# Kernel tuning notes

Measured on AMD Instinct MI355X. Metric: run time of the kernel, lower is better.

The kernel has to match this reference:

```python
import jax, jax.numpy as jnp
import numpy as np

M = 64            # multiplicity of 0e and of 1e irreps
NM = 2 * M        # num_mul = 128
SQ3 = float(np.sqrt(3.0))
SQ6 = float(np.sqrt(6.0))
C0 = float(np.sqrt(1.0 / 5.0))   # path weight for 0e outputs: sqrt(dim_out=1 / n_paths=5)
C1 = float(np.sqrt(3.0 / 5.0))   # path weight for 1e outputs: sqrt(dim_out=3 / n_paths=5)


def split_irreps(x):
    # x: [..., 256] -> scalars [..., 64], vectors [..., 64, 3]
    return x[:, :M], x[:, M:].reshape(x.shape[0], M, 3)


def merge_irreps(s, v):
    return jnp.concatenate([s, v.reshape(v.shape[0], -1)], axis=-1)


def o3_linear(x, W0, b0, W1):
    # e3nn o3.Linear: per-l mixing across multiplicities, shared over m, 1/sqrt(fan_in) norm, bias only on 0e
    s, v = split_irreps(x)
    s = s @ W0 / jnp.sqrt(jnp.float32(M)) + b0
    v = jnp.einsum('nuc,uv->nvc', v, W1) / jnp.sqrt(jnp.float32(M))
    return merge_irreps(s, v)


def ssp(x):
    return jax.nn.softplus(x) - jnp.log(2.0)


def norm_gate(x, W1, b1, W2, b2):
    # NormGate: gate 1e channels by MLP of [scalars, per-channel norms]
    s, v = split_irreps(x)
    nrm = jnp.sqrt(jnp.sum(v * v, axis=-1))             # [E, M]
    f0 = jnp.concatenate([s, nrm], axis=-1)             # [E, 2M]
    g = jax.nn.silu(f0 @ W1 + b1) @ W2 + b2             # [E, 2M]
    return merge_irreps(g[:, :M], v * g[:, M:, None])


def tp_node_pair(x, y, w):
    # weighted 'uuu' tensor product, instructions: (0e,0e->0e), (0e,1e->1e), (1e,0e->1e), (1e,1e->0e), (1e,1e->1e)
    xs, xv = split_irreps(x)
    ys, yv = split_irreps(y)
    w000, w011, w101, w110, w111 = jnp.split(w, 5, axis=-1)   # each [E, M]
    out_s = C0 * (w000 * xs * ys + w110 * jnp.sum(xv * yv, -1) / SQ3)
    out_v = C1 * (w011[..., None] * xs[..., None] * yv / SQ3
                  + w101[..., None] * xv * ys[..., None] / SQ3
                  + w111[..., None] * jnp.cross(xv, yv) / SQ6)
    return merge_irreps(out_s, out_v)


def reference(node_attr, edge_attr, node_pair_attr, Wi0, bi0, Wi1, gpW1, gpb1, gpW2, gpb2,
              Wn0, bn0, Wn1, feW1, feW2, fsW1, fsb1, fsW2, fsb2,
              gW1, gb1, gW2, gb2, Wo0, bo0, Wo1, edge_index):
    dst, src = edge_index[0], edge_index[1]
    # --- invariant branch: per-edge scalar descriptor s0 ---
    na0 = o3_linear(node_attr, Wi0, bi0, Wi1)
    s_d, v_d = split_irreps(na0[dst])
    s_s, v_s = split_irreps(na0[src])
    ip = jnp.sum(v_d * v_s, axis=-1) / 3.0               # InnerProduct of 1e channels (1/ir.dim)
    s0 = jnp.concatenate([s_d, s_s, ip], axis=-1)        # [E, 3M]
    # --- node feature branch ---
    h = norm_gate(node_attr, gpW1, gpb1, gpW2, gpb2)
    h = o3_linear(h, Wn0, bn0, Wn1)
    # --- edge-conditioned TP weights ---
    fe = ssp(edge_attr @ feW1 / jnp.sqrt(32.0)) @ feW2 / jnp.sqrt(8.0)   # FullyConnectedNet, [E, 5M]
    fs = jax.nn.silu(s0 @ fsW1 + fsb1) @ fsW2 + fsb2                     # [E, 5M]
    w = fe * fs
    # --- pair message ---
    pair = tp_node_pair(h[src], h[dst], w)
    pair = norm_gate(pair, gW1, gb1, gW2, gb2)
    pair = o3_linear(pair, Wo0, bo0, Wo1)
    return pair + node_pair_attr


def setup_inputs():
    key = jax.random.key(0)
    ks = jax.random.split(key, 20)
    N, E, EA, WN = 20000, 120000, 32, 320
    f32 = jnp.float32
    def nrm(k, shape, scale=1.0):
        return jax.random.normal(k, shape, dtype=f32) * scale
    return {
        'node_attr': nrm(ks[0], (N, 4 * M)),
        'edge_attr': nrm(ks[1], (E, EA)),
        'node_pair_attr': nrm(ks[2], (E, 4 * M)),
        'Wi0': nrm(ks[3], (M, M)), 'bi0': jnp.zeros((M,), f32), 'Wi1': nrm(ks[4], (M, M)),
        'gpW1': nrm(ks[5], (NM, NM), 1.0 / np.sqrt(NM)), 'gpb1': jnp.zeros((NM,), f32),
        'gpW2': nrm(ks[6], (NM, NM), 1.0 / np.sqrt(NM)), 'gpb2': jnp.zeros((NM,), f32),
        'Wn0': nrm(ks[7], (M, M)), 'bn0': jnp.zeros((M,), f32), 'Wn1': nrm(ks[8], (M, M)),
        'feW1': nrm(ks[9], (EA, 8)), 'feW2': nrm(ks[10], (8, WN)),
        'fsW1': nrm(ks[11], (3 * M, M), 1.0 / np.sqrt(3 * M)), 'fsb1': jnp.zeros((M,), f32),
        'fsW2': nrm(ks[12], (M, WN), 1.0 / np.sqrt(M)), 'fsb2': jnp.zeros((WN,), f32),
        'gW1': nrm(ks[13], (NM, NM), 1.0 / np.sqrt(NM)), 'gb1': jnp.zeros((NM,), f32),
        'gW2': nrm(ks[14], (NM, NM), 1.0 / np.sqrt(NM)), 'gb2': jnp.zeros((NM,), f32),
        'Wo0': nrm(ks[15], (M, M)), 'bo0': jnp.zeros((M,), f32), 'Wo1': nrm(ks[16], (M, M)),
        'edge_index': jax.random.randint(ks[17], (2, E), 0, N, dtype=jnp.int32),
    }
```

## Files before the change

kernel.cpp:

```cpp
#include <hip/hip_runtime.h>
#include <hip/hip_bf16.h>
#include <math.h>


static __device__ __forceinline__ float siluf(float x) { return x / (1.f + __expf(-x)); }
static __device__ __forceinline__ float sspf(float x) {
  return fmaxf(x, 0.f) + log1pf(__expf(-fabsf(x))) - 0.6931471805599453f;
}
static __device__ __forceinline__ short f2b(float x) {
  __hip_bfloat16 b = __float2bfloat16(x);
  short s; __builtin_memcpy(&s, &b, 2); return s;
}
static __device__ __forceinline__ float b2f(short s) {
  unsigned int u = ((unsigned int)(unsigned short)s) << 16;
  float f; __builtin_memcpy(&f, &u, 4); return f;
}

typedef __attribute__((ext_vector_type(4))) short short4v;
typedef __attribute__((ext_vector_type(8))) short short8v;
typedef __attribute__((ext_vector_type(16))) float f32x16;

static __device__ __forceinline__ short8v ld8(const short* p) {
  const short4v* q = (const short4v*)p;
  short4v a = q[0], b = q[1];
  short8v r;
  r[0] = a[0]; r[1] = a[1]; r[2] = a[2]; r[3] = a[3];
  r[4] = b[0]; r[5] = b[1]; r[6] = b[2]; r[7] = b[3];
  return r;
}

static __device__ __forceinline__ short8v gld8(const short* __restrict__ p) {
  return *reinterpret_cast<const short8v*>(p);
}

static __device__ __forceinline__ void sp2(short* hp, short* lp, float x) {
  short hh = f2b(x); *hp = hh; *lp = f2b(x - b2f(hh));
}

#define WOFF_FSW1 0
#define WOFF_FSW2 12288
#define WOFF_FEW1 32768
#define WOFF_FEW2 33792
#define WOFF_GW1  38912
#define WOFF_GW2  55296
#define WOFF_WO0  71680
#define WOFF_WO1  75776
#define NOFF_WI0  79872
#define NOFF_WI1  88064
#define NOFF_GP1  96256
#define NOFF_GP2  129024
#define NOFF_WN0  161792
#define NOFF_WN1  169984
#define W_ALL     178176

__global__ __launch_bounds__(256) void prep_weights(
    const float* __restrict__ fsW1, const float* __restrict__ fsW2,
    const float* __restrict__ feW1, const float* __restrict__ feW2,
    const float* __restrict__ gW1, const float* __restrict__ gW2,
    const float* __restrict__ Wo0, const float* __restrict__ Wo1,
    const float* __restrict__ Wi0, const float* __restrict__ Wi1,
    const float* __restrict__ gpW1, const float* __restrict__ gpW2,
    const float* __restrict__ Wn0, const float* __restrict__ Wn1,
    short* __restrict__ wsb)
{
  const int gt = blockIdx.x * blockDim.x + threadIdx.x;
  const int gs = gridDim.x * blockDim.x;
  for (int i = gt; i < 12288; i += gs) { int k = (i >> 10) * 16 + (i & 15), n = (i >> 4) & 63;  wsb[WOFF_FSW1 + i] = f2b(fsW1[k * 64 + n]); }
  for (int i = gt; i < 20480; i += gs) { int k = (i / 5120) * 16 + (i & 15), n = (i >> 4) % 320; wsb[WOFF_FSW2 + i] = f2b(fsW2[k * 320 + n]); }
  for (int i = gt; i < 1024; i += gs)  { int k = (i >> 9) * 16 + (i & 15),  n = (i >> 4) & 31;  wsb[WOFF_FEW1 + i] = (n < 8) ? f2b(feW1[k * 8 + n]) : 0; }
  for (int i = gt; i < 5120; i += gs)  { int k = i & 15,                    n = (i >> 4) % 320; wsb[WOFF_FEW2 + i] = (k < 8) ? f2b(feW2[k * 320 + n]) : 0; }
  for (int i = gt; i < 16384; i += gs) { int k = (i >> 11) * 16 + (i & 15), n = (i >> 4) & 127; wsb[WOFF_GW1 + i] = f2b(gW1[k * 128 + n]); }
  for (int i = gt; i < 16384; i += gs) { int k = (i >> 11) * 16 + (i & 15), n = (i >> 4) & 127; wsb[WOFF_GW2 + i] = f2b(gW2[k * 128 + n]); }
  for (int i = gt; i < 4096; i += gs)  { int k = (i >> 10) * 16 + (i & 15), n = (i >> 4) & 63;  wsb[WOFF_WO0 + i] = f2b(Wo0[k * 64 + n]); }
  for (int i = gt; i < 4096; i += gs)  { int k = (i >> 10) * 16 + (i & 15), n = (i >> 4) & 63;  wsb[WOFF_WO1 + i] = f2b(Wo1[k * 64 + n]); }
  for (int i = gt; i < 4096; i += gs)  { int k = (i >> 10) * 16 + (i & 15), n = (i >> 4) & 63;  float w = Wi0[k * 64 + n];  short hh = f2b(w); wsb[NOFF_WI0 + i] = hh; wsb[NOFF_WI0 + 4096 + i] = f2b(w - b2f(hh)); }
  for (int i = gt; i < 4096; i += gs)  { int k = (i >> 10) * 16 + (i & 15), n = (i >> 4) & 63;  float w = Wi1[k * 64 + n];  short hh = f2b(w); wsb[NOFF_WI1 + i] = hh; wsb[NOFF_WI1 + 4096 + i] = f2b(w - b2f(hh)); }
  for (int i = gt; i < 16384; i += gs) { int k = (i >> 11) * 16 + (i & 15), n = (i >> 4) & 127; float w = gpW1[k * 128 + n]; short hh = f2b(w); wsb[NOFF_GP1 + i] = hh; wsb[NOFF_GP1 + 16384 + i] = f2b(w - b2f(hh)); }
  for (int i = gt; i < 16384; i += gs) { int k = (i >> 11) * 16 + (i & 15), n = (i >> 4) & 127; float w = gpW2[k * 128 + n]; short hh = f2b(w); wsb[NOFF_GP2 + i] = hh; wsb[NOFF_GP2 + 16384 + i] = f2b(w - b2f(hh)); }
  for (int i = gt; i < 4096; i += gs)  { int k = (i >> 10) * 16 + (i & 15), n = (i >> 4) & 63;  float w = Wn0[k * 64 + n];  short hh = f2b(w); wsb[NOFF_WN0 + i] = hh; wsb[NOFF_WN0 + 4096 + i] = f2b(w - b2f(hh)); }
  for (int i = gt; i < 4096; i += gs)  { int k = (i >> 10) * 16 + (i & 15), n = (i >> 4) & 63;  float w = Wn1[k * 64 + n];  short hh = f2b(w); wsb[NOFF_WN1 + i] = hh; wsb[NOFF_WN1 + 4096 + i] = f2b(w - b2f(hh)); }
}

#define MFMA32(a, b, c) __builtin_amdgcn_mfma_f32_32x32x16_bf16(a, b, c, 0, 0, 0)

#define MFMA_HL(ah, al, bh, bl, acc) \
  do { acc = MFMA32((al), (bh), acc); acc = MFMA32((ah), (bl), acc); acc = MFMA32((ah), (bh), acc); } while (0)

#define XS_H 0
#define V0H  4352
#define F0H  17408
#define F0L  21632
#define TBH  0
#define TBL  4224
#define GVH  8704
#define GSH  21760
#define GSL  23936
#define NODE_LDS_SHORTS 26112

__global__ __launch_bounds__(256, 2) void node_kernel(
    const float* __restrict__ na,
    const float* __restrict__ bi0, const float* __restrict__ gpb1,
    const float* __restrict__ gpb2, const float* __restrict__ bn0,
    const short* __restrict__ wsb,
    float* __restrict__ na0, float* __restrict__ h, int N)
{
  __shared__ __align__(16) short smem[NODE_LDS_SHORTS];
  const int tid = threadIdx.x;
  const int wv = tid >> 6, ln = tid & 63;
  const int m32 = ln & 31, kh = ln >> 5;
  const int nb0 = blockIdx.x * 32;

  for (int i = 0; i < 8; ++i) {
    const int e = wv * 8 + i;
    int ng = nb0 + e; if (ng >= N) ng = N - 1;
    const float* xp = na + (size_t)ng * 256;
    const int u = ln;
    const float xs = xp[u];
    const float v0 = xp[64 + 3 * u], v1 = xp[64 + 3 * u + 1], v2 = xp[64 + 3 * u + 2];
    const float nr = sqrtf(v0 * v0 + v1 * v1 + v2 * v2);
    sp2(smem + XS_H + e * 68 + u,        smem + XS_H + 2176 + e * 68 + u, xs);
    sp2(smem + V0H + 0 * 4352 + e * 68 + u, smem + V0H + 0 * 4352 + 2176 + e * 68 + u, v0);
    sp2(smem + V0H + 1 * 4352 + e * 68 + u, smem + V0H + 1 * 4352 + 2176 + e * 68 + u, v1);
    sp2(smem + V0H + 2 * 4352 + e * 68 + u, smem + V0H + 2 * 4352 + 2176 + e * 68 + u, v2);
    sp2(smem + F0H + e * 132 + u,        smem + F0L + e * 132 + u, xs);
    sp2(smem + F0H + e * 132 + 64 + u,   smem + F0L + e * 132 + 64 + u, nr);
  }
  __syncthreads();

  {
    const int g = wv;
    const short* Ah = smem + (g == 0 ? XS_H : V0H + (g - 1) * 4352) + m32 * 68 + kh * 8;
    const short* Al = Ah + 2176;
    const int bofs = (g == 0) ? NOFF_WI0 : NOFF_WI1;
    for (int nt = 0; nt < 2; ++nt) {
      f32x16 acc = {};
      const int n = nt * 32 + m32;
      const short* Bh = wsb + bofs + n * 16 + kh * 8;
      const short* Bl = Bh + 4096;
#pragma unroll 2
      for (int k0 = 0; k0 < 4; ++k0) {
        short8v ah = ld8(Ah + k0 * 16), al = ld8(Al + k0 * 16);
        short8v bh = gld8(Bh + k0 * 1024), bl = gld8(Bl + k0 * 1024);
        MFMA_HL(ah, al, bh, bl, acc);
      }
      const float bias = (g == 0) ? bi0[n] : 0.f;
      const int off = (g == 0) ? n : 64 + 3 * n + (g - 1);
#pragma unroll
      for (int r = 0; r < 16; ++r) {
        int row = (r & 3) + 8 * (r >> 2) + 4 * kh;
        int ng = nb0 + row;
        if (ng < N) na0[(size_t)ng * 256 + off] = acc[r] * 0.125f + bias;
      }
    }
  }
  __syncthreads();

  {
    f32x16 acc = {};
    const int n = wv * 32 + m32;
    const short* Ah = smem + F0H + m32 * 132 + kh * 8;
    const short* Al = smem + F0L + m32 * 132 + kh * 8;
    const short* Bh = wsb + NOFF_GP1 + n * 16 + kh * 8;
    const short* Bl = Bh + 16384;
#pragma unroll 2
    for (int k0 = 0; k0 < 8; ++k0) {
      short8v ah = ld8(Ah + k0 * 16), al = ld8(Al + k0 * 16);
      short8v bh = gld8(Bh + k0 * 2048), bl = gld8(Bl + k0 * 2048);
      MFMA_HL(ah, al, bh, bl, acc);
    }
    const float bias = gpb1[n];
#pragma unroll
    for (int r = 0; r < 16; ++r) {
      int row = (r & 3) + 8 * (r >> 2) + 4 * kh;
      float t = siluf(acc[r] + bias);
      sp2(smem + TBH + row * 132 + n, smem + TBL + row * 132 + n, t);
    }
  }
  __syncthreads();

  {
    f32x16 acc = {};
    const int n = wv * 32 + m32;
    const short* Ah = smem + TBH + m32 * 132 + kh * 8;
    const short* Al = smem + TBL + m32 * 132 + kh * 8;
    const short* Bh = wsb + NOFF_GP2 + n * 16 + kh * 8;
    const short* Bl = Bh + 16384;
#pragma unroll 2
    for (int k0 = 0; k0 < 8; ++k0) {
      short8v ah = ld8(Ah + k0 * 16), al = ld8(Al + k0 * 16);
      short8v bh = gld8(Bh + k0 * 2048), bl = gld8(Bl + k0 * 2048);
      MFMA_HL(ah, al, bh, bl, acc);
    }
    const float bias = gpb2[n];
#pragma unroll
    for (int r = 0; r < 16; ++r) {
      int row = (r & 3) + 8 * (r >> 2) + 4 * kh;
      float val = acc[r] + bias;
      if (wv < 2) {
        sp2(smem + GSH + row * 68 + n, smem + GSL + row * 68 + n, val);
      } else {
        const int u = n - 64;
        int ng = nb0 + row; if (ng >= N) ng = N - 1;
        const float* vp = na + (size_t)ng * 256 + 64 + 3 * u;
#pragma unroll
        for (int c = 0; c < 3; ++c) {
          float pv = vp[c] * val;
          sp2(smem + GVH + c * 4352 + row * 68 + u,
              smem + GVH + c * 4352 + 2176 + row * 68 + u, pv);
        }
      }
    }
  }
  __syncthreads();

  {
    const int g = wv;
    const short* Ah = smem + (g == 0 ? GSH : GVH + (g - 1) * 4352) + m32 * 68 + kh * 8;
    const short* Al = Ah + 2176;
    const int bofs = (g == 0) ? NOFF_WN0 : NOFF_WN1;
    for (int nt = 0; nt < 2; ++nt) {
      f32x16 acc = {};
      const int n = nt * 32 + m32;
      const short* Bh = wsb + bofs + n * 16 + kh * 8;
      const short* Bl = Bh + 4096;
#pragma unroll 2
      for (int k0 = 0; k0 < 4; ++k0) {
        short8v ah = ld8(Ah + k0 * 16), al = ld8(Al + k0 * 16);
        short8v bh = gld8(Bh + k0 * 1024), bl = gld8(Bl + k0 * 1024);
        MFMA_HL(ah, al, bh, bl, acc);
      }
      const float bias = (g == 0) ? bn0[n] : 0.f;
      const int off = (g == 0) ? n : 64 + 3 * n + (g - 1);
#pragma unroll
      for (int r = 0; r < 16; ++r) {
        int row = (r & 3) + 8 * (r >> 2) + 4 * kh;
        int ng = nb0 + row;
        if (ng < N) h[(size_t)ng * 256 + off] = acc[r] * 0.125f + bias;
      }
    }
  }
}

#define A_HIDE  0
#define A_HID2  640
#define A_S0    2816
#define A_EA    9088
#define A_WB    2816
#define A_F0    13056
#define A_PV    17280
#define A_TB    2816
#define A_GATED 7040
#define ACT_TOTAL 23424
#define LDS_BYTES (ACT_TOTAL * 2)

__global__ __launch_bounds__(256, 3) void edge_kernel(
    const float* __restrict__ ea,
    const float* __restrict__ npa,
    const float* __restrict__ fsb1, const float* __restrict__ fsb2,
    const float* __restrict__ gb1, const float* __restrict__ gb2,
    const float* __restrict__ bo0,
    const int* __restrict__ eidx,
    const float* __restrict__ na0, const float* __restrict__ h,
    const short* __restrict__ wsb,
    float* __restrict__ out, int E)
{
  extern __shared__ __align__(16) short smem[];
  short* hidEb  = smem + A_HIDE;
  short* hid2b  = smem + A_HID2;
  short* s0b    = smem + A_S0;
  short* earowb = smem + A_EA;
  short* wb     = smem + A_WB;
  short* f0b    = smem + A_F0;
  short* pvb    = smem + A_PV;
  short* tb     = smem + A_TB;
  short* gated  = smem + A_GATED;

  const int tid = threadIdx.x;
  const int wv = tid >> 6, ln = tid & 63;
  const int m32 = ln & 31, kh = ln >> 5;
  const int e0 = blockIdx.x * 32;

  const float C0c = 0.4472135954999579f;
  const float C1c = 0.7745966692414834f;
  const float iS3 = 0.5773502691896258f;
  const float iS6 = 0.40824829046386307f;
  const float isq32 = 0.17677669529663687f;
  const float isq8 = 0.35355339059327373f;

  for (int i = tid; i < 32 * 32; i += 256) {
    int e = i >> 5, k = i & 31;
    int eg = e0 + e; if (eg >= E) eg = E - 1;
    earowb[e * 36 + k] = f2b(ea[(size_t)eg * 32 + k]);
  }
  for (int i = tid; i < 640; i += 256) hidEb[i] = 0;
  for (int i = 0; i < 8; ++i) {
    int e = wv * 8 + i;
    int eg = e0 + e; if (eg >= E) eg = E - 1;
    const int dst = eidx[eg], src = eidx[E + eg];
    const float* nd = na0 + (size_t)dst * 256;
    const float* ns = na0 + (size_t)src * 256;
    const int u = ln;
    float ip = nd[64 + 3 * u] * ns[64 + 3 * u] + nd[64 + 3 * u + 1] * ns[64 + 3 * u + 1]
             + nd[64 + 3 * u + 2] * ns[64 + 3 * u + 2];
    s0b[e * 196 + u] = f2b(nd[u]);
    s0b[e * 196 + 64 + u] = f2b(ns[u]);
    s0b[e * 196 + 128 + u] = f2b(ip * (1.f / 3.f));
  }
  __syncthreads();

  if (wv < 2) {
    f32x16 acc = {};
    const int n = wv * 32 + m32;
    const short* A = s0b + m32 * 196 + kh * 8;
    const short* B = wsb + WOFF_FSW1 + n * 16 + kh * 8;
#pragma unroll
    for (int k0 = 0; k0 < 12; ++k0)
      acc = MFMA32(ld8(A + k0 * 16), gld8(B + k0 * 1024), acc);
    const float bias = fsb1[n];
#pragma unroll
    for (int r = 0; r < 16; ++r) {
      int row = (r & 3) + 8 * (r >> 2) + 4 * kh;
      hid2b[row * 68 + n] = f2b(siluf(acc[r] + bias));
    }
  } else if (wv == 2) {
    f32x16 acc = {};
    const short* A = earowb + m32 * 36 + kh * 8;
    const short* B = wsb + WOFF_FEW1 + m32 * 16 + kh * 8;
#pragma unroll
    for (int k0 = 0; k0 < 2; ++k0)
      acc = MFMA32(ld8(A + k0 * 16), gld8(B + k0 * 512), acc);
    if (m32 < 8) {
#pragma unroll
      for (int r = 0; r < 16; ++r) {
        int row = (r & 3) + 8 * (r >> 2) + 4 * kh;
        hidEb[row * 20 + m32] = f2b(sspf(acc[r] * isq32));
      }
    }
  }
  __syncthreads();

  for (int nt = wv; nt < 10; nt += 4) {
    f32x16 acc = {};
    const int n = nt * 32 + m32;
    acc = MFMA32(ld8(hidEb + m32 * 20 + kh * 8), gld8(wsb + WOFF_FEW2 + n * 16 + kh * 8), acc);
#pragma unroll
    for (int r = 0; r < 16; ++r) {
      int row = (r & 3) + 8 * (r >> 2) + 4 * kh;
      wb[row * 320 + n] = f2b(acc[r] * isq8);
    }
  }
  __syncthreads();

  for (int nt = wv; nt < 10; nt += 4) {
    f32x16 acc = {};
    const int n = nt * 32 + m32;
    const short* A = hid2b + m32 * 68 + kh * 8;
    const short* B = wsb + WOFF_FSW2 + n * 16 + kh * 8;
#pragma unroll
    for (int k0 = 0; k0 < 4; ++k0)
      acc = MFMA32(ld8(A + k0 * 16), gld8(B + k0 * 5120), acc);
    const float bias = fsb2[n];
#pragma unroll
    for (int r = 0; r < 16; ++r) {
      int row = (r & 3) + 8 * (r >> 2) + 4 * kh;
      float fsv = acc[r] + bias;
      wb[row * 320 + n] = f2b(fsv * b2f(wb[row * 320 + n]));
    }
  }
  __syncthreads();

  for (int i = 0; i < 8; ++i) {
    int e = wv * 8 + i;
    int eg = e0 + e; if (eg >= E) eg = E - 1;
    const int dst = eidx[eg], src = eidx[E + eg];
    const float* hs = h + (size_t)src * 256;
    const float* hd = h + (size_t)dst * 256;
    const int u = ln;
    const float w0 = b2f(wb[e * 320 + u]);
    const float w1 = b2f(wb[e * 320 + u + 64]);
    const float w2 = b2f(wb[e * 320 + u + 128]);
    const float w3 = b2f(wb[e * 320 + u + 192]);
    const float w4 = b2f(wb[e * 320 + u + 256]);
    const float xs = hs[u], ys = hd[u];
    const float xv0 = hs[64 + 3 * u], xv1 = hs[64 + 3 * u + 1], xv2 = hs[64 + 3 * u + 2];
    const float yv0 = hd[64 + 3 * u], yv1 = hd[64 + 3 * u + 1], yv2 = hd[64 + 3 * u + 2];
    const float ipv = xv0 * yv0 + xv1 * yv1 + xv2 * yv2;
    const float cr0 = xv1 * yv2 - xv2 * yv1;
    const float cr1 = xv2 * yv0 - xv0 * yv2;
    const float cr2 = xv0 * yv1 - xv1 * yv0;
    const float ps = C0c * (w0 * xs * ys + w3 * ipv * iS3);
    const float k011 = C1c * iS3 * w1 * xs;
    const float k101 = C1c * iS3 * w2 * ys;
    const float k111 = C1c * iS6 * w4;
    const float pv0 = k011 * yv0 + k101 * xv0 + k111 * cr0;
    const float pv1 = k011 * yv1 + k101 * xv1 + k111 * cr1;
    const float pv2 = k011 * yv2 + k101 * xv2 + k111 * cr2;
    f0b[e * 132 + u] = f2b(ps);
    f0b[e * 132 + 64 + u] = f2b(sqrtf(pv0 * pv0 + pv1 * pv1 + pv2 * pv2));
    pvb[e * 192 + 3 * u + 0] = f2b(pv0);
    pvb[e * 192 + 3 * u + 1] = f2b(pv1);
    pvb[e * 192 + 3 * u + 2] = f2b(pv2);
  }
  __syncthreads();

  {
    f32x16 acc = {};
    const int n = wv * 32 + m32;
    const short* A = f0b + m32 * 132 + kh * 8;
    const short* B = wsb + WOFF_GW1 + n * 16 + kh * 8;
#pragma unroll
    for (int k0 = 0; k0 < 8; ++k0)
      acc = MFMA32(ld8(A + k0 * 16), gld8(B + k0 * 2048), acc);
    const float bias = gb1[n];
#pragma unroll
    for (int r = 0; r < 16; ++r) {
      int row = (r & 3) + 8 * (r >> 2) + 4 * kh;
      tb[row * 132 + n] = f2b(siluf(acc[r] + bias));
    }
  }
  __syncthreads();

  {
    f32x16 acc = {};
    const int n = wv * 32 + m32;
    const short* A = tb + m32 * 132 + kh * 8;
    const short* B = wsb + WOFF_GW2 + n * 16 + kh * 8;
#pragma unroll
    for (int k0 = 0; k0 < 8; ++k0)
      acc = MFMA32(ld8(A + k0 * 16), gld8(B + k0 * 2048), acc);
    const float bias = gb2[n];
#pragma unroll
    for (int r = 0; r < 16; ++r) {
      int row = (r & 3) + 8 * (r >> 2) + 4 * kh;
      float val = acc[r] + bias;
      if (wv < 2) {
        gated[row * 68 + n] = f2b(val);
      } else {
        int u = n - 64;
        float p0 = b2f(pvb[row * 192 + 3 * u + 0]);
        float p1 = b2f(pvb[row * 192 + 3 * u + 1]);
        float p2 = b2f(pvb[row * 192 + 3 * u + 2]);
        gated[2176 * 1 + row * 68 + u] = f2b(p0 * val);
        gated[2176 * 2 + row * 68 + u] = f2b(p1 * val);
        gated[2176 * 3 + row * 68 + u] = f2b(p2 * val);
      }
    }
  }
  __syncthreads();

  {
    const short* A = gated + 2176 * wv + m32 * 68 + kh * 8;
    const int bofs = (wv == 0) ? WOFF_WO0 : WOFF_WO1;
    for (int nt = 0; nt < 2; ++nt) {
      f32x16 acc = {};
      const int n = nt * 32 + m32;
      const short* B = wsb + bofs + n * 16 + kh * 8;
#pragma unroll
      for (int k0 = 0; k0 < 4; ++k0)
        acc = MFMA32(ld8(A + k0 * 16), gld8(B + k0 * 1024), acc);
      const float bias = (wv == 0) ? bo0[n] : 0.f;
      const int off = (wv == 0) ? n : 64 + 3 * n + (wv - 1);
#pragma unroll
      for (int r = 0; r < 16; ++r) {
        int row = (r & 3) + 8 * (r >> 2) + 4 * kh;
        int eg = e0 + row;
        if (eg < E)
          out[(size_t)eg * 256 + off] = acc[r] * 0.125f + bias + npa[(size_t)eg * 256 + off];
      }
    }
  }
}

extern "C" void kernel_launch(void* const* d_in, const int* in_sizes, int n_in,
                              void* d_out, int out_size, void* d_ws, size_t ws_size,
                              hipStream_t stream) {
  const float* node_attr = (const float*)d_in[0];
  const float* edge_attr = (const float*)d_in[1];
  const float* npa  = (const float*)d_in[2];
  const float* Wi0  = (const float*)d_in[3];
  const float* bi0  = (const float*)d_in[4];
  const float* Wi1  = (const float*)d_in[5];
  const float* gpW1 = (const float*)d_in[6];
  const float* gpb1 = (const float*)d_in[7];
  const float* gpW2 = (const float*)d_in[8];
  const float* gpb2 = (const float*)d_in[9];
  const float* Wn0  = (const float*)d_in[10];
  const float* bn0  = (const float*)d_in[11];
  const float* Wn1  = (const float*)d_in[12];
  const float* feW1 = (const float*)d_in[13];
  const float* feW2 = (const float*)d_in[14];
  const float* fsW1 = (const float*)d_in[15];
  const float* fsb1 = (const float*)d_in[16];
  const float* fsW2 = (const float*)d_in[17];
  const float* fsb2 = (const float*)d_in[18];
  const float* gW1  = (const float*)d_in[19];
  const float* gb1  = (const float*)d_in[20];
  const float* gW2  = (const float*)d_in[21];
  const float* gb2  = (const float*)d_in[22];
  const float* Wo0  = (const float*)d_in[23];
  const float* bo0  = (const float*)d_in[24];
  const float* Wo1  = (const float*)d_in[25];
  const int* eidx = (const int*)d_in[26];

  const int N = in_sizes[0] / 256;
  const int E = in_sizes[1] / 32;

  float* na0 = (float*)d_ws;
  float* h = na0 + (size_t)N * 256;
  short* wsb = (short*)(h + (size_t)N * 256);

  (void)hipFuncSetAttribute((const void*)edge_kernel,
                            hipFuncAttributeMaxDynamicSharedMemorySize,
                            LDS_BYTES);

  prep_weights<<<96, 256, 0, stream>>>(fsW1, fsW2, feW1, feW2, gW1, gW2, Wo0, Wo1,
                                       Wi0, Wi1, gpW1, gpW2, Wn0, Wn1, wsb);
  node_kernel<<<(N + 31) / 32, 256, 0, stream>>>(node_attr, bi0, gpb1, gpb2, bn0,
                                                 wsb, na0, h, N);
  edge_kernel<<<(E + 31) / 32, 256, LDS_BYTES, stream>>>(
      edge_attr, npa, fsb1, fsb2, gb1, gb2, bo0, eidx, na0, h, wsb, (float*)d_out, E);
}
```

Measured before the change: 502.8 us.

## Prefetch gathered node features and residual early, fuse edge-weight GEMM stages

Edge indices and the gathered h features for each wave's 8 edges are loaded into registers at kernel start, and the npa residual values are loaded before the gate GEMMs. This lets the global-memory latency of these gathers overlap with earlier compute instead of stalling later phases. The two edge-weight GEMM loops are also fused into one, which removes a barrier and an LDS read-modify-write round trip. The cost is much higher register pressure (around 100 extra floats per thread), which may reduce occupancy or cause spills.

```diff
diff --git a/kernel.cpp b/kernel.cpp
--- a/kernel.cpp
+++ b/kernel.cpp
@@ -287,18 +287,40 @@
   const float isq32 = 0.17677669529663687f;
   const float isq8 = 0.35355339059327373f;
 
+  int dstI[8], srcI[8];
+#pragma unroll
+  for (int i = 0; i < 8; ++i) {
+    int eg = e0 + wv * 8 + i; if (eg >= E) eg = E - 1;
+    dstI[i] = eidx[eg]; srcI[i] = eidx[E + eg];
+  }
+
+  float hs_s[8], hd_s[8];
+  float hs_v0[8], hs_v1[8], hs_v2[8], hd_v0[8], hd_v1[8], hd_v2[8];
+#pragma unroll
+  for (int i = 0; i < 8; ++i) {
+    const float* hs = h + (size_t)srcI[i] * 256;
+    const float* hd = h + (size_t)dstI[i] * 256;
+    hs_s[i] = hs[ln];
+    hd_s[i] = hd[ln];
+    hs_v0[i] = hs[64 + 3 * ln];
+    hs_v1[i] = hs[64 + 3 * ln + 1];
+    hs_v2[i] = hs[64 + 3 * ln + 2];
+    hd_v0[i] = hd[64 + 3 * ln];
+    hd_v1[i] = hd[64 + 3 * ln + 1];
+    hd_v2[i] = hd[64 + 3 * ln + 2];
+  }
+
   for (int i = tid; i < 32 * 32; i += 256) {
     int e = i >> 5, k = i & 31;
     int eg = e0 + e; if (eg >= E) eg = E - 1;
     earowb[e * 36 + k] = f2b(ea[(size_t)eg * 32 + k]);
   }
   for (int i = tid; i < 640; i += 256) hidEb[i] = 0;
+#pragma unroll
   for (int i = 0; i < 8; ++i) {
-    int e = wv * 8 + i;
-    int eg = e0 + e; if (eg >= E) eg = E - 1;
-    const int dst = eidx[eg], src = eidx[E + eg];
-    const float* nd = na0 + (size_t)dst * 256;
-    const float* ns = na0 + (size_t)src * 256;
+    const int e = wv * 8 + i;
+    const float* nd = na0 + (size_t)dstI[i] * 256;
+    const float* ns = na0 + (size_t)srcI[i] * 256;
     const int u = ln;
     float ip = nd[64 + 3 * u] * ns[64 + 3 * u] + nd[64 + 3 * u + 1] * ns[64 + 3 * u + 1]
              + nd[64 + 3 * u + 2] * ns[64 + 3 * u + 2];
@@ -340,50 +362,36 @@
   __syncthreads();
 
   for (int nt = wv; nt < 10; nt += 4) {
-    f32x16 acc = {};
     const int n = nt * 32 + m32;
-    acc = MFMA32(ld8(hidEb + m32 * 20 + kh * 8), gld8(wsb + WOFF_FEW2 + n * 16 + kh * 8), acc);
+    f32x16 aF = {};
+    aF = MFMA32(ld8(hidEb + m32 * 20 + kh * 8), gld8(wsb + WOFF_FEW2 + n * 16 + kh * 8), aF);
+    f32x16 aS = {};
+    const short* A = hid2b + m32 * 68 + kh * 8;
+    const short* B = wsb + WOFF_FSW2 + n * 16 + kh * 8;
+#pragma unroll
+    for (int k0 = 0; k0 < 4; ++k0)
+      aS = MFMA32(ld8(A + k0 * 16), gld8(B + k0 * 5120), aS);
+    const float bias = fsb2[n];
 #pragma unroll
     for (int r = 0; r < 16; ++r) {
       int row = (r & 3) + 8 * (r >> 2) + 4 * kh;
-      wb[row * 320 + n] = f2b(acc[r] * isq8);
-    }
-  }
-  __syncthreads();
-
-  for (int nt = wv; nt < 10; nt += 4) {
-    f32x16 acc = {};
-    const int n = nt * 32 + m32;
-    const short* A = hid2b + m32 * 68 + kh * 8;
-    const short* B = wsb + WOFF_FSW2 + n * 16 + kh * 8;
-#pragma unroll
-    for (int k0 = 0; k0 < 4; ++k0)
-      acc = MFMA32(ld8(A + k0 * 16), gld8(B + k0 * 5120), acc);
-    const float bias = fsb2[n];
-#pragma unroll
-    for (int r = 0; r < 16; ++r) {
-      int row = (r & 3) + 8 * (r >> 2) + 4 * kh;
-      float fsv = acc[r] + bias;
-      wb[row * 320 + n] = f2b(fsv * b2f(wb[row * 320 + n]));
-    }
-  }
-  __syncthreads();
-
+      wb[row * 320 + n] = f2b((aS[r] + bias) * (aF[r] * isq8));
+    }
+  }
+  __syncthreads();
+
+#pragma unroll
   for (int i = 0; i < 8; ++i) {
-    int e = wv * 8 + i;
-    int eg = e0 + e; if (eg >= E) eg = E - 1;
-    const int dst = eidx[eg], src = eidx[E + eg];
-    const float* hs = h + (size_t)src * 256;
-    const float* hd = h + (size_t)dst * 256;
+    const int e = wv * 8 + i;
     const int u = ln;
     const float w0 = b2f(wb[e * 320 + u]);
     const float w1 = b2f(wb[e * 320 + u + 64]);
     const float w2 = b2f(wb[e * 320 + u + 128]);
     const float w3 = b2f(wb[e * 320 + u + 192]);
     const float w4 = b2f(wb[e * 320 + u + 256]);
-    const float xs = hs[u], ys = hd[u];
-    const float xv0 = hs[64 + 3 * u], xv1 = hs[64 + 3 * u + 1], xv2 = hs[64 + 3 * u + 2];
-    const float yv0 = hd[64 + 3 * u], yv1 = hd[64 + 3 * u + 1], yv2 = hd[64 + 3 * u + 2];
+    const float xs = hs_s[i], ys = hd_s[i];
+    const float xv0 = hs_v0[i], xv1 = hs_v1[i], xv2 = hs_v2[i];
+    const float yv0 = hd_v0[i], yv1 = hd_v1[i], yv2 = hd_v2[i];
     const float ipv = xv0 * yv0 + xv1 * yv1 + xv2 * yv2;
     const float cr0 = xv1 * yv2 - xv2 * yv1;
     const float cr1 = xv2 * yv0 - xv0 * yv2;
@@ -420,6 +428,20 @@
   }
   __syncthreads();
 
+  float npv[2][16];
+  {
+#pragma unroll
+    for (int nt = 0; nt < 2; ++nt) {
+      const int n = nt * 32 + m32;
+      const int off = (wv == 0) ? n : 64 + 3 * n + (wv - 1);
+#pragma unroll
+      for (int r = 0; r < 16; ++r) {
+        int row = (r & 3) + 8 * (r >> 2) + 4 * kh;
+        int eg = e0 + row;
+        npv[nt][r] = (eg < E) ? npa[(size_t)eg * 256 + off] : 0.f;
+      }
+    }
+  }
   {
     f32x16 acc = {};
     const int n = wv * 32 + m32;
@@ -451,6 +473,7 @@
   {
     const short* A = gated + 2176 * wv + m32 * 68 + kh * 8;
     const int bofs = (wv == 0) ? WOFF_WO0 : WOFF_WO1;
+#pragma unroll
     for (int nt = 0; nt < 2; ++nt) {
       f32x16 acc = {};
       const int n = nt * 32 + m32;
@@ -465,7 +488,7 @@
         int row = (r & 3) + 8 * (r >> 2) + 4 * kh;
         int eg = e0 + row;
         if (eg < E)
-          out[(size_t)eg * 256 + off] = acc[r] * 0.125f + bias + npa[(size_t)eg * 256 + off];
+          out[(size_t)eg * 256 + off] = acc[r] * 0.125f + bias + npv[nt][r];
       }
     }
   }
```

After: 437.8 us. -12.9%, faster.
